# Kernel optimization log

Hardware: AMD Instinct MI355X
Metric: run time of the kernel (lower is better)

## Reference

```python
import jax, jax.numpy as jnp
import numpy as np

KNOW, ITEM, D, L, LAT, B, S = 1024, 20000, 128, 2, 256, 256, 200
NTOT = ITEM + KNOW
E1, E2 = 32768, 160000


def graph_layer(h, W, a, src, dst, n):
    # GAT-style: gather src/dst, edge MLP, segment softmax over dst, weighted scatter-sum
    z = h @ W                                              # [N, D]
    e = jax.nn.leaky_relu((jnp.concatenate([z[src], z[dst]], axis=-1) @ a)[:, 0])  # [E]
    m = jax.ops.segment_max(e, dst, num_segments=n)
    m = jnp.where(jnp.isfinite(m), m, 0.0)                 # nodes with no in-edges
    w = jnp.exp(e - m[dst])                                # [E]
    den = jax.ops.segment_sum(w, dst, num_segments=n)      # [N]
    num = jax.ops.segment_sum(w[:, None] * z[src], dst, num_segments=n)  # [N, D]
    return jnp.where(den[:, None] > 0, num / jnp.maximum(den, 1e-12)[:, None], 0.0)


def setup_inputs() -> dict:
    key = jax.random.key(0)
    ks = jax.random.split(key, 32)
    p = lambda i, shp: jax.random.normal(ks[i], shp, dtype=jnp.float32) * 0.05
    inp = {
        'p_rec': jax.random.randint(ks[0], (B, S), 0, ITEM),
        'p_target': jax.random.randint(ks[1], (B,), 0, S),
        'a_rec': jax.random.randint(ks[2], (B, S), 0, 3),
        'kn_rec': jax.random.uniform(ks[3], (B, S, KNOW), dtype=jnp.float32),
        'kn_num': jnp.ones((B, S), dtype=jnp.float32),
        'src1': jax.random.randint(ks[4], (E1,), 0, KNOW),
        'dst1': jax.random.randint(ks[5], (E1,), 0, KNOW),
        'src2': jax.random.randint(ks[6], (E2,), 0, NTOT),
        'dst2': jax.random.randint(ks[7], (E2,), 0, NTOT),
        'src3': jax.random.randint(ks[8], (E2,), 0, NTOT),
        'dst3': jax.random.randint(ks[9], (E2,), 0, NTOT),
        'kn_table': p(10, (KNOW, D)),
        'exer_table': p(11, (ITEM, D)),
        'ans_table': p(12, (3, D)),
        'gW': p(13, (L, 3, D, D)),
        'gA': p(14, (L, 3, 2 * D, 1)),
        'raW1': p(15, (L, D, D)),
        'raB1': jnp.zeros((L, D), jnp.float32),
        'raW2': p(16, (L, D, 1)),
        'actW1': p(17, (3 * D, LAT)),
        'actB1': jnp.zeros((LAT,), jnp.float32),
        'actW2': p(18, (LAT, ITEM)),
        'actB2': jnp.zeros((ITEM,), jnp.float32),
        'vW1': p(19, (3, 3 * D, LAT)),
        'vB1': jnp.zeros((3, LAT), jnp.float32),
        'vW2': p(20, (3, LAT, 1)),
        'vB2': jnp.zeros((3, 1), jnp.float32),
    }
    return inp


def reference(p_rec, p_target, a_rec, kn_rec, kn_num, src1, dst1, src2, dst2, src3, dst3,
              kn_table, exer_table, ans_table, gW, gA, raW1, raB1, raW2,
              actW1, actB1, actW2, actB2, vW1, vB1, vW2, vB2):
    kn, ex = kn_table, exer_table
    for l in range(L):  # GraphEncoder: stacked Fusion blocks (distinct params)
        k_dir = graph_layer(kn, gW[l, 0], gA[l, 0], src1, dst1, KNOW)
        ek = jnp.concatenate([ex, kn], axis=0)             # [NTOT, D]
        kfe = graph_layer(ek, gW[l, 1], gA[l, 1], src2, dst2, NTOT)
        efk = graph_layer(ek, gW[l, 2], gA[l, 2], src3, dst3, NTOT)
        A_, B_ = k_dir, kfe[ITEM:]
        ra = lambda x: jnp.tanh(x @ raW1[l] + raB1[l]) @ raW2[l]  # [KNOW, 1]
        s = jax.nn.softmax(jnp.concatenate([ra(A_), ra(B_)], axis=1), axis=1)
        kn = s[:, :1] * A_ + s[:, 1:2] * B_
        ex = efk[:ITEM]
    # hidden_layer
    be = ex[p_rec]                                         # [B, S, D]
    ba = ans_table[a_rec]                                  # [B, S, D]
    bk = jnp.einsum('bsk,kd->bsd', kn_rec, kn) / kn_num[..., None]
    item = jnp.concatenate([be, ba, bk], axis=-1)          # [B, S, 3D]
    m = (jnp.arange(S)[None, :] < (p_target + 1)[:, None]).astype(item.dtype)
    h = (item * m[..., None]).sum(axis=1) / m.sum(axis=1, keepdims=True)  # [B, 3D]
    logits = jnp.tanh(h @ actW1 + actB1) @ actW2 + actB2   # [B, ITEM]
    vh = jnp.tanh(jnp.einsum('bd,kdl->kbl', h, vW1) + vB1[:, None, :])
    vals = jnp.einsum('kbl,klo->kbo', vh, vW2) + vB2[:, None, :]  # [3, B, 1]
    return logits, vals[0], vals[1], vals[2]
```

## Files before the change

### kernel.cpp

```cpp
#include <hip/hip_runtime.h>

#define D 128
#define KNOW 1024
#define ITEM 20000
#define NTOT (ITEM + KNOW)
#define LAYERS 2
#define LAT 256
#define BB 256
#define SS 200
#define H3 (3 * D)
#define CH 4
#define ZROWS 64
#define NBK (KNOW / ZROWS)
#define NBN ((NTOT + ZROWS - 1) / ZROWS)
#define NZT (NBK + NBN)
#define NAGGU (KNOW / 4 + ITEM / 4)
#define NKROW (BB * CH)
#define XPITCH 68
#define NLOGB ((ITEM + 255) / 256)
#define NLV (NLOGB * (BB / 32))
#define NVB ((3 * BB + 3) / 4)

__global__ __launch_bounds__(256) void zdv_ker(
    const float* __restrict__ Xe, const float* __restrict__ Xk,
    const float* __restrict__ gW, const float* __restrict__ gA,
    const float* __restrict__ wa2, int layer,
    float* __restrict__ z1, float* __restrict__ z3,
    float* __restrict__ ds1, float* __restrict__ dd1,
    float* __restrict__ ds2, float* __restrict__ dd2,
    float* __restrict__ ds3, float* __restrict__ dd3)
{
    __shared__ __align__(16) float xT[D * XPITCH];
    int bid = blockIdx.x;
    int g, row0, nmax;
    if (bid < NBK) { g = 0; row0 = bid * ZROWS;          nmax = KNOW; }
    else           { g = 2; row0 = (bid - NBK) * ZROWS;  nmax = NTOT; }
    const float* W = gW + (size_t)(layer * 3 + g) * D * D;
    const float* A = gA + (size_t)(layer * 3 + g) * 2 * D;
    float* Z  = (g == 0) ? z1  : z3;
    float* DS = (g == 0) ? ds1 : ds3;
    float* DD = (g == 0) ? dd1 : dd3;

    int tid = threadIdx.x;
#pragma unroll
    for (int i = 0; i < 8; ++i) {
        int flat = tid + i * 256;
        int row  = flat >> 5;
        int f4   = flat & 31;
        int grow = row0 + row;
        float4 v = make_float4(0.f, 0.f, 0.f, 0.f);
        if (grow < nmax) {
            const float* src = (g == 0) ? (Xk + (size_t)grow * D)
                             : (grow < ITEM ? Xe + (size_t)grow * D
                                            : Xk + (size_t)(grow - ITEM) * D);
            v = *(const float4*)(src + f4 * 4);
        }
        int slot = row ^ ((f4 & 7) << 2);
        int kk = f4 * 4;
        xT[(kk + 0) * XPITCH + slot] = v.x;
        xT[(kk + 1) * XPITCH + slot] = v.y;
        xT[(kk + 2) * XPITCH + slot] = v.z;
        xT[(kk + 3) * XPITCH + slot] = v.w;
    }
    __syncthreads();

    int cg_ = tid & 31;
    int rg = tid >> 5;
    int c0 = cg_ * 4;
    int r0a = rg * 8, r0b = rg * 8 + 4;

    float acc[8][4];
#pragma unroll
    for (int r = 0; r < 8; ++r)
#pragma unroll
        for (int c = 0; c < 4; ++c) acc[r][c] = 0.f;

#pragma unroll 4
    for (int k = 0; k < D; ++k) {
        float4 wv = *(const float4*)(W + (size_t)k * D + c0);
        int xc = ((k >> 2) & 7) << 2;
        float4 xa = *(const float4*)&xT[k * XPITCH + (r0a ^ xc)];
        float4 xb = *(const float4*)&xT[k * XPITCH + (r0b ^ xc)];
        acc[0][0] = fmaf(xa.x, wv.x, acc[0][0]); acc[0][1] = fmaf(xa.x, wv.y, acc[0][1]);
        acc[0][2] = fmaf(xa.x, wv.z, acc[0][2]); acc[0][3] = fmaf(xa.x, wv.w, acc[0][3]);
        acc[1][0] = fmaf(xa.y, wv.x, acc[1][0]); acc[1][1] = fmaf(xa.y, wv.y, acc[1][1]);
        acc[1][2] = fmaf(xa.y, wv.z, acc[1][2]); acc[1][3] = fmaf(xa.y, wv.w, acc[1][3]);
        acc[2][0] = fmaf(xa.z, wv.x, acc[2][0]); acc[2][1] = fmaf(xa.z, wv.y, acc[2][1]);
        acc[2][2] = fmaf(xa.z, wv.z, acc[2][2]); acc[2][3] = fmaf(xa.z, wv.w, acc[2][3]);
        acc[3][0] = fmaf(xa.w, wv.x, acc[3][0]); acc[3][1] = fmaf(xa.w, wv.y, acc[3][1]);
        acc[3][2] = fmaf(xa.w, wv.z, acc[3][2]); acc[3][3] = fmaf(xa.w, wv.w, acc[3][3]);
        acc[4][0] = fmaf(xb.x, wv.x, acc[4][0]); acc[4][1] = fmaf(xb.x, wv.y, acc[4][1]);
        acc[4][2] = fmaf(xb.x, wv.z, acc[4][2]); acc[4][3] = fmaf(xb.x, wv.w, acc[4][3]);
        acc[5][0] = fmaf(xb.y, wv.x, acc[5][0]); acc[5][1] = fmaf(xb.y, wv.y, acc[5][1]);
        acc[5][2] = fmaf(xb.y, wv.z, acc[5][2]); acc[5][3] = fmaf(xb.y, wv.w, acc[5][3]);
        acc[6][0] = fmaf(xb.z, wv.x, acc[6][0]); acc[6][1] = fmaf(xb.z, wv.y, acc[6][1]);
        acc[6][2] = fmaf(xb.z, wv.z, acc[6][2]); acc[6][3] = fmaf(xb.z, wv.w, acc[6][3]);
        acc[7][0] = fmaf(xb.w, wv.x, acc[7][0]); acc[7][1] = fmaf(xb.w, wv.y, acc[7][1]);
        acc[7][2] = fmaf(xb.w, wv.z, acc[7][2]); acc[7][3] = fmaf(xb.w, wv.w, acc[7][3]);
    }

#pragma unroll
    for (int r = 0; r < 8; ++r) {
        int grow = row0 + ((r < 4) ? (r0a + r) : (r0b + r - 4));
        if (grow < nmax) {
            float4 v = make_float4(acc[r][0], acc[r][1], acc[r][2], acc[r][3]);
            *(float4*)(Z + (size_t)grow * D + c0) = v;
        }
    }

    float4 as = *(const float4*)(A + c0);
    float4 ad = *(const float4*)(A + D + c0);
    float ps[8], pd[8];
#pragma unroll
    for (int r = 0; r < 8; ++r) {
        ps[r] = acc[r][0] * as.x + acc[r][1] * as.y + acc[r][2] * as.z + acc[r][3] * as.w;
        pd[r] = acc[r][0] * ad.x + acc[r][1] * ad.y + acc[r][2] * ad.z + acc[r][3] * ad.w;
    }
#pragma unroll
    for (int m = 16; m; m >>= 1) {
#pragma unroll
        for (int r = 0; r < 8; ++r) {
            ps[r] += __shfl_xor(ps[r], m, 64);
            pd[r] += __shfl_xor(pd[r], m, 64);
        }
    }
    if (cg_ == 0) {
#pragma unroll
        for (int r = 0; r < 8; ++r) {
            int grow = row0 + ((r < 4) ? (r0a + r) : (r0b + r - 4));
            if (grow < nmax) { DS[grow] = ps[r]; DD[grow] = pd[r]; }
        }
    }

    if (g == 2) {
        const float* was = wa2 + (size_t)layer * 2 * D;
        float4 ws4 = *(const float4*)(was + c0);
        float4 wd4 = *(const float4*)(was + D + c0);
        int xc = ((c0 >> 2) & 7) << 2;
        float pxs[8], pxd[8];
#pragma unroll
        for (int r = 0; r < 8; ++r) {
            int rr = (r < 4) ? (r0a + r) : (r0b + r - 4);
            int sl = rr ^ xc;
            float x0 = xT[(c0 + 0) * XPITCH + sl];
            float x1 = xT[(c0 + 1) * XPITCH + sl];
            float x2 = xT[(c0 + 2) * XPITCH + sl];
            float x3 = xT[(c0 + 3) * XPITCH + sl];
            pxs[r] = x0 * ws4.x + x1 * ws4.y + x2 * ws4.z + x3 * ws4.w;
            pxd[r] = x0 * wd4.x + x1 * wd4.y + x2 * wd4.z + x3 * wd4.w;
        }
#pragma unroll
        for (int m = 16; m; m >>= 1) {
#pragma unroll
            for (int r = 0; r < 8; ++r) {
                pxs[r] += __shfl_xor(pxs[r], m, 64);
                pxd[r] += __shfl_xor(pxd[r], m, 64);
            }
        }
        if (cg_ == 0) {
#pragma unroll
            for (int r = 0; r < 8; ++r) {
                int grow = row0 + ((r < 4) ? (r0a + r) : (r0b + r - 4));
                if (grow < nmax) { ds2[grow] = pxs[r]; dd2[grow] = pxd[r]; }
            }
        }
    }
}

__global__ void hist3(const int* __restrict__ d1, const int* __restrict__ d2, const int* __restrict__ d3,
                      int E1, int E2, int* __restrict__ c1, int* __restrict__ c2, int* __restrict__ c3) {
    int i = blockIdx.x * blockDim.x + threadIdx.x;
    if (i < E1) atomicAdd(&c1[d1[i]], 1);
    else if (i < E1 + E2) { int d = d2[i - E1]; if (d >= ITEM) atomicAdd(&c2[d - ITEM], 1); }
    else if (i < E1 + 2 * E2) { int d = d3[i - E1 - E2]; if (d < ITEM) atomicAdd(&c3[d], 1); }
}

__global__ __launch_bounds__(1024) void exscan3(int* __restrict__ c1, int* __restrict__ o1,
                                                int* __restrict__ c2, int* __restrict__ o2,
                                                int* __restrict__ c3, int* __restrict__ o3,
                                                const float* __restrict__ gW, const float* __restrict__ gA,
                                                float* __restrict__ wa2) {
    int g = blockIdx.x;
    if (g == 3) {
        int t = threadIdx.x;
        if (t < 2 * 2 * D) {
            int l = t >> 8, rem = t & 255;
            int v = rem >> 7, k = rem & 127;
            const float* Wp = gW + (size_t)(l * 3 + 1) * D * D + (size_t)k * D;
            const float* ap = gA + (size_t)(l * 3 + 1) * 2 * D + v * D;
            float s = 0.f;
#pragma unroll 4
            for (int j = 0; j < D; ++j) s = fmaf(Wp[j], ap[j], s);
            wa2[(l * 2 + v) * D + k] = s;
        }
        return;
    }
    int* cnt = (g == 0) ? c1 : (g == 1 ? c2 : c3);
    int* off = (g == 0) ? o1 : (g == 1 ? o2 : o3);
    int n = (g == 2) ? ITEM : KNOW;
    int tid = threadIdx.x, lane = tid & 63, wid = tid >> 6;
    int L = (n + 1023) >> 10;
    int i0 = tid * L;
    int sum = 0;
    for (int q = 0; q < L; ++q) {
        int i = i0 + q;
        if (i < n) sum += cnt[i];
    }
    int x = sum;
#pragma unroll
    for (int d = 1; d < 64; d <<= 1) { int t = __shfl_up(x, d, 64); if (lane >= d) x += t; }
    __shared__ int ws[16];
    if (lane == 63) ws[wid] = x;
    __syncthreads();
    if (wid == 0) {
        int w = (lane < 16) ? ws[lane] : 0;
#pragma unroll
        for (int d = 1; d < 16; d <<= 1) { int t = __shfl_up(w, d, 64); if (lane >= d) w += t; }
        if (lane < 16) ws[lane] = w;
    }
    __syncthreads();
    int run = x - sum + ((wid > 0) ? ws[wid - 1] : 0);
    if (tid == 0) off[0] = 0;
    for (int q = 0; q < L; ++q) {
        int i = i0 + q;
        if (i < n) {
            int v = cnt[i];
            cnt[i] = run;
            run += v;
            off[i + 1] = run;
        }
    }
}

__global__ void scatter3(const int* __restrict__ s1, const int* __restrict__ d1,
                         const int* __restrict__ s2, const int* __restrict__ d2,
                         const int* __restrict__ s3, const int* __restrict__ d3,
                         int E1, int E2, int* __restrict__ cur1, int* __restrict__ cur2, int* __restrict__ cur3,
                         int* __restrict__ e1, int* __restrict__ e2, int* __restrict__ e3) {
    int i = blockIdx.x * blockDim.x + threadIdx.x;
    if (i < E1) { int p = atomicAdd(&cur1[d1[i]], 1); e1[p] = s1[i]; }
    else if (i < E1 + E2) { int j = i - E1; int d = d2[j]; if (d >= ITEM) { int p = atomicAdd(&cur2[d - ITEM], 1); e2[p] = s2[j]; } }
    else if (i < E1 + 2 * E2) { int j = i - E1 - E2; int d = d3[j]; if (d < ITEM) { int p = atomicAdd(&cur3[d], 1); e3[p] = s3[j]; } }
}

__device__ __forceinline__ void agg_row(const float* __restrict__ Z, const float* __restrict__ dsrc,
                                        float dd, const int* __restrict__ es, int e0, int e1,
                                        int lane, float* __restrict__ acc) {
#pragma unroll
    for (int q = 0; q < 8; ++q) acc[q] = 0.f;
    if (e1 <= e0) return;
    int eg = lane >> 4, cs = lane & 15;
    float den = 0.f;
#pragma unroll 2
    for (int e = e0 + eg; e < e1; e += 4) {
        int s = es[e];
        float t = dsrc[s] + dd;
        t = (t > 0.f) ? t : 0.01f * t;
        float w = __expf(t);
        den += w;
        const float4* zr = (const float4*)(Z + (size_t)s * D + cs * 8);
        float4 za = zr[0], zb = zr[1];
        acc[0] = fmaf(w, za.x, acc[0]); acc[1] = fmaf(w, za.y, acc[1]);
        acc[2] = fmaf(w, za.z, acc[2]); acc[3] = fmaf(w, za.w, acc[3]);
        acc[4] = fmaf(w, zb.x, acc[4]); acc[5] = fmaf(w, zb.y, acc[5]);
        acc[6] = fmaf(w, zb.z, acc[6]); acc[7] = fmaf(w, zb.w, acc[7]);
    }
#pragma unroll
    for (int m = 16; m <= 32; m <<= 1) {
        den += __shfl_xor(den, m, 64);
#pragma unroll
        for (int q = 0; q < 8; ++q) acc[q] += __shfl_xor(acc[q], m, 64);
    }
    float inv = 1.f / fmaxf(den, 1e-12f);
#pragma unroll
    for (int q = 0; q < 8; ++q) acc[q] *= inv;
}

__device__ __forceinline__ void agg_rowX(const float* __restrict__ Xe, const float* __restrict__ Xk,
                                         const float* __restrict__ dsrc, float dd,
                                         const int* __restrict__ es, int e0, int e1,
                                         int lane, float* __restrict__ acc) {
#pragma unroll
    for (int q = 0; q < 8; ++q) acc[q] = 0.f;
    if (e1 <= e0) return;
    int eg = lane >> 4, cs = lane & 15;
    float den = 0.f;
#pragma unroll 2
    for (int e = e0 + eg; e < e1; e += 4) {
        int s = es[e];
        float t = dsrc[s] + dd;
        t = (t > 0.f) ? t : 0.01f * t;
        float w = __expf(t);
        den += w;
        const float* xr = (s < ITEM) ? (Xe + (size_t)s * D) : (Xk + (size_t)(s - ITEM) * D);
        const float4* zr = (const float4*)(xr + cs * 8);
        float4 za = zr[0], zb = zr[1];
        acc[0] = fmaf(w, za.x, acc[0]); acc[1] = fmaf(w, za.y, acc[1]);
        acc[2] = fmaf(w, za.z, acc[2]); acc[3] = fmaf(w, za.w, acc[3]);
        acc[4] = fmaf(w, zb.x, acc[4]); acc[5] = fmaf(w, zb.y, acc[5]);
        acc[6] = fmaf(w, zb.z, acc[6]); acc[7] = fmaf(w, zb.w, acc[7]);
    }
#pragma unroll
    for (int m = 16; m <= 32; m <<= 1) {
        den += __shfl_xor(den, m, 64);
#pragma unroll
        for (int q = 0; q < 8; ++q) acc[q] += __shfl_xor(acc[q], m, 64);
    }
    float inv = 1.f / fmaxf(den, 1e-12f);
#pragma unroll
    for (int q = 0; q < 8; ++q) acc[q] *= inv;
}

__global__ __launch_bounds__(256) void agg3c(
    const float* __restrict__ Xe, const float* __restrict__ Xk,
    const float* __restrict__ z1, const float* __restrict__ z3,
    const float* __restrict__ ds1, const float* __restrict__ dd1,
    const float* __restrict__ ds2, const float* __restrict__ dd2,
    const float* __restrict__ ds3, const float* __restrict__ dd3,
    const int* __restrict__ off1, const int* __restrict__ es1,
    const int* __restrict__ off2, const int* __restrict__ es2,
    const int* __restrict__ off3, const int* __restrict__ es3,
    const float* __restrict__ gW1L,
    const float* __restrict__ raW1L, const float* __restrict__ raB1L,
    const float* __restrict__ raW2L, float* __restrict__ out,
    const float* __restrict__ kn_rec, const float* __restrict__ kn_num,
    const int* __restrict__ p_target, float* __restrict__ krowP)
{
    int wv = threadIdx.x >> 6, lane = threadIdx.x & 63;
    int eg = lane >> 4, cs = lane & 15;
    int u = blockIdx.x;
    if (u < KNOW / 4) {
        __shared__ float ABs[4][2][D];
        __shared__ float Bf[4][D];
        int i = u * 4 + wv;
        float accA[8], accB[8];
        agg_row(z1, ds1, dd1[i], es1, off1[i], off1[i + 1], lane, accA);
        agg_rowX(Xe, Xk, ds2, dd2[ITEM + i], es2, off2[i], off2[i + 1], lane, accB);
        if (eg == 0) {
            *(float4*)&ABs[wv][0][cs * 8]     = make_float4(accA[0], accA[1], accA[2], accA[3]);
            *(float4*)&ABs[wv][0][cs * 8 + 4] = make_float4(accA[4], accA[5], accA[6], accA[7]);
            *(float4*)&ABs[wv][1][cs * 8]     = make_float4(accB[0], accB[1], accB[2], accB[3]);
            *(float4*)&ABs[wv][1][cs * 8 + 4] = make_float4(accB[4], accB[5], accB[6], accB[7]);
        }
        __syncthreads();
        int j0 = lane * 2;
        float fB0 = 0.f, fB1 = 0.f;
#pragma unroll 4
        for (int k = 0; k < D; ++k) {
            float xv = ABs[wv][1][k];
            float2 w = *(const float2*)(gW1L + (size_t)k * D + j0);
            fB0 = fmaf(xv, w.x, fB0); fB1 = fmaf(xv, w.y, fB1);
        }
        Bf[wv][j0] = fB0; Bf[wv][j0 + 1] = fB1;
        __syncthreads();
        float b0 = raB1L[j0], b1 = raB1L[j0 + 1];
        float aA0 = b0, aA1 = b1, aB0 = b0, aB1 = b1;
#pragma unroll 4
        for (int k = 0; k < D; ++k) {
            float av = ABs[wv][0][k], bv = Bf[wv][k];
            float2 w = *(const float2*)(raW1L + (size_t)k * D + j0);
            aA0 = fmaf(av, w.x, aA0); aA1 = fmaf(av, w.y, aA1);
            aB0 = fmaf(bv, w.x, aB0); aB1 = fmaf(bv, w.y, aB1);
        }
        float2 w2 = *(const float2*)(raW2L + j0);
        float pA = tanhf(aA0) * w2.x + tanhf(aA1) * w2.y;
        float pB = tanhf(aB0) * w2.x + tanhf(aB1) * w2.y;
#pragma unroll
        for (int o = 32; o; o >>= 1) { pA += __shfl_xor(pA, o, 64); pB += __shfl_xor(pB, o, 64); }
        float mx2 = fmaxf(pA, pB);
        float eA = __expf(pA - mx2), eB = __expf(pB - mx2);
        float s = 1.f / (eA + eB);
        float sA = eA * s, sB = eB * s;
        float2 Av = *(float2*)&ABs[wv][0][j0];
        float2 Bv = make_float2(Bf[wv][j0], Bf[wv][j0 + 1]);
        *(float2*)(out + (size_t)(ITEM + i) * D + j0) =
            make_float2(sA * Av.x + sB * Bv.x, sA * Av.y + sB * Bv.y);
    } else if (u < NAGGU) {
        int row = (u - KNOW / 4) * 4 + wv;
        if (row < ITEM) {
            float acc[8];
            agg_row(z3, ds3, dd3[row], es3, off3[row], off3[row + 1], lane, acc);
            if (eg == 0) {
                *(float4*)(out + (size_t)row * D + cs * 8)     = make_float4(acc[0], acc[1], acc[2], acc[3]);
                *(float4*)(out + (size_t)row * D + cs * 8 + 4) = make_float4(acc[4], acc[5], acc[6], acc[7]);
            }
        }
    } else {
        int uk = u - NAGGU;
        int b = uk & (BB - 1), ch = uk >> 8;
        int cnt = p_target[b] + 1;
        int per = (SS + CH - 1) / CH;
        int s0 = ch * per, s1 = s0 + per;
        if (s1 > cnt) s1 = cnt;
        int k0 = threadIdx.x * 4;
        float4 a = make_float4(0.f, 0.f, 0.f, 0.f);
        for (int s = s0; s < s1; ++s) {
            float inv = 1.f / kn_num[b * SS + s];
            float4 v = *(const float4*)(kn_rec + ((size_t)b * SS + s) * KNOW + k0);
            a.x += v.x * inv; a.y += v.y * inv; a.z += v.z * inv; a.w += v.w * inv;
        }
        *(float4*)(krowP + ((size_t)ch * BB + b) * KNOW + k0) = a;
    }
}

__global__ __launch_bounds__(512) void hker(const float* __restrict__ ex, const float* __restrict__ ans_table,
                                            const int* __restrict__ p_rec, const int* __restrict__ a_rec,
                                            const int* __restrict__ p_target, const float* __restrict__ krowP,
                                            const float* __restrict__ kn, float* __restrict__ h) {
    int b = blockIdx.x;
    int j = threadIdx.x & 127, sg = threadIdx.x >> 7;
    int cnt = p_target[b] + 1;
    __shared__ int pidx[SS], aidx[SS];
    __shared__ float kr[KNOW];
    __shared__ float red[4][3][128];
    for (int i = threadIdx.x; i < cnt; i += 512) { pidx[i] = p_rec[b * SS + i]; aidx[i] = a_rec[b * SS + i]; }
    for (int i = threadIdx.x; i < KNOW; i += 512) {
        float s = 0.f;
#pragma unroll
        for (int c = 0; c < CH; ++c) s += krowP[((size_t)c * BB + b) * KNOW + i];
        kr[i] = s;
    }
    __syncthreads();
    float accE = 0.f, accA = 0.f;
    for (int s = sg; s < cnt; s += 4) {
        accE += ex[(size_t)pidx[s] * D + j];
        accA += ans_table[aidx[s] * D + j];
    }
    float accK = 0.f;
    for (int k = sg * 256; k < sg * 256 + 256; ++k) accK += kr[k] * kn[(size_t)k * D + j];
    red[sg][0][j] = accE; red[sg][1][j] = accA; red[sg][2][j] = accK;
    __syncthreads();
    if (sg == 0) {
        float inv = 1.f / (float)cnt;
        float e = (red[0][0][j] + red[1][0][j] + red[2][0][j] + red[3][0][j]) * inv;
        float a = (red[0][1][j] + red[1][1][j] + red[2][1][j] + red[3][1][j]) * inv;
        float kv = (red[0][2][j] + red[1][2][j] + red[2][2][j] + red[3][2][j]) * inv;
        h[b * H3 + j] = e;
        h[b * H3 + D + j] = a;
        h[b * H3 + 2 * D + j] = kv;
    }
}

__global__ __launch_bounds__(256) void hidden_gemm(const float* __restrict__ h,
                                                   const float* __restrict__ actW1, const float* __restrict__ actB1,
                                                   const float* __restrict__ vW1, const float* __restrict__ vB1,
                                                   float* __restrict__ hid) {
    __shared__ float hT[H3 * 17];
    int tid = threadIdx.x;
    int b0 = blockIdx.x * 16;
    for (int idx = tid; idx < 16 * H3; idx += 256) {
        int r = idx / H3, k = idx - r * H3;
        hT[k * 17 + r] = h[(size_t)(b0 + r) * H3 + k];
    }
    __syncthreads();
    int j = blockIdx.y * 64 + (tid & 63);
    int head = j >> 8, jj = j & 255;
    int rg = tid >> 6, r0 = rg * 4;
    const float* W = (head == 0) ? actW1 : (vW1 + (size_t)(head - 1) * H3 * LAT);
    float bias = (head == 0) ? actB1[jj] : vB1[(head - 1) * LAT + jj];
    float acc[4] = {bias, bias, bias, bias};
#pragma unroll 4
    for (int k = 0; k < H3; ++k) {
        float w = W[(size_t)k * LAT + jj];
        float h0 = hT[k * 17 + r0 + 0];
        float h1 = hT[k * 17 + r0 + 1];
        float h2 = hT[k * 17 + r0 + 2];
        float h3 = hT[k * 17 + r0 + 3];
        acc[0] = fmaf(h0, w, acc[0]);
        acc[1] = fmaf(h1, w, acc[1]);
        acc[2] = fmaf(h2, w, acc[2]);
        acc[3] = fmaf(h3, w, acc[3]);
    }
#pragma unroll
    for (int r = 0; r < 4; ++r)
        hid[((size_t)head * BB + (b0 + r0 + r)) * LAT + jj] = tanhf(acc[r]);
}

__global__ __launch_bounds__(256) void logitsvals(const float* __restrict__ hid,
                                                  const float* __restrict__ actW2, const float* __restrict__ actB2,
                                                  const float* __restrict__ vW2, const float* __restrict__ vB2,
                                                  float* __restrict__ out) {
    int bid = blockIdx.x;
    int tid = threadIdx.x;
    if (bid < NLV) {
        __shared__ float hT[LAT * 33];
        int ix = bid / (BB / 32), iy = bid % (BB / 32);
        int b0 = iy * 32;
        for (int idx = tid; idx < 32 * LAT; idx += 256) {
            int r = idx >> 8, k = idx & 255;
            hT[k * 33 + r] = hid[(size_t)(b0 + r) * LAT + k];
        }
        __syncthreads();
        int lane6 = tid & 63;
        int rg = tid >> 6, r0 = rg * 8;
        int ibase = ix * 256 + lane6;
        int icol[4], icl[4];
        float bias[4];
#pragma unroll
        for (int c = 0; c < 4; ++c) {
            icol[c] = ibase + c * 64;
            icl[c] = icol[c] < ITEM ? icol[c] : (ITEM - 1);
            bias[c] = actB2[icl[c]];
        }
        float acc[8][4];
#pragma unroll
        for (int r = 0; r < 8; ++r)
#pragma unroll
            for (int c = 0; c < 4; ++c) acc[r][c] = bias[c];
#pragma unroll 2
        for (int k = 0; k < LAT; ++k) {
            float w0 = actW2[(size_t)k * ITEM + icl[0]];
            float w1 = actW2[(size_t)k * ITEM + icl[1]];
            float w2 = actW2[(size_t)k * ITEM + icl[2]];
            float w3 = actW2[(size_t)k * ITEM + icl[3]];
            const float* hp = &hT[k * 33 + r0];
#pragma unroll
            for (int r = 0; r < 8; ++r) {
                float hv = hp[r];
                acc[r][0] = fmaf(hv, w0, acc[r][0]);
                acc[r][1] = fmaf(hv, w1, acc[r][1]);
                acc[r][2] = fmaf(hv, w2, acc[r][2]);
                acc[r][3] = fmaf(hv, w3, acc[r][3]);
            }
        }
#pragma unroll
        for (int c = 0; c < 4; ++c) {
            if (icol[c] < ITEM) {
#pragma unroll
                for (int r = 0; r < 8; ++r)
                    out[(size_t)(b0 + r0 + r) * ITEM + icol[c]] = acc[r][c];
            }
        }
    } else {
        int idx = (bid - NLV) * 4 + (tid >> 6);
        int lane = tid & 63;
        if (idx >= 3 * BB) return;
        int k = idx / BB, b = idx - k * BB;
        const float* vh = hid + ((size_t)(k + 1) * BB + b) * LAT;
        float4 a = ((const float4*)vh)[lane];
        float4 w = ((const float4*)(vW2 + k * LAT))[lane];
        float s = a.x * w.x + a.y * w.y + a.z * w.z + a.w * w.w;
#pragma unroll
        for (int o = 32; o; o >>= 1) s += __shfl_down(s, o, 64);
        if (lane == 0) out[(size_t)BB * ITEM + k * BB + b] = s + vB2[k];
    }
}

extern "C" void kernel_launch(void* const* d_in, const int* in_sizes, int n_in,
                              void* d_out, int out_size, void* d_ws, size_t ws_size,
                              hipStream_t stream) {
    const int*   p_rec      = (const int*)d_in[0];
    const int*   p_target   = (const int*)d_in[1];
    const int*   a_rec      = (const int*)d_in[2];
    const float* kn_rec     = (const float*)d_in[3];
    const float* kn_num     = (const float*)d_in[4];
    const int*   src1       = (const int*)d_in[5];
    const int*   dst1       = (const int*)d_in[6];
    const int*   src2       = (const int*)d_in[7];
    const int*   dst2       = (const int*)d_in[8];
    const int*   src3       = (const int*)d_in[9];
    const int*   dst3       = (const int*)d_in[10];
    const float* kn_table   = (const float*)d_in[11];
    const float* exer_table = (const float*)d_in[12];
    const float* ans_table  = (const float*)d_in[13];
    const float* gW         = (const float*)d_in[14];
    const float* gA         = (const float*)d_in[15];
    const float* raW1       = (const float*)d_in[16];
    const float* raB1       = (const float*)d_in[17];
    const float* raW2       = (const float*)d_in[18];
    const float* actW1      = (const float*)d_in[19];
    const float* actB1      = (const float*)d_in[20];
    const float* actW2      = (const float*)d_in[21];
    const float* actB2      = (const float*)d_in[22];
    const float* vW1        = (const float*)d_in[23];
    const float* vB1        = (const float*)d_in[24];
    const float* vW2        = (const float*)d_in[25];
    const float* vB2        = (const float*)d_in[26];
    const int E1 = in_sizes[5], E2 = in_sizes[7];

    float* base = (float*)d_ws;
    size_t o = 0;
    auto alloc = [&](size_t n) -> float* { float* p = base + o; o += (n + 3) & ~(size_t)3; return p; };
    float* buf0 = alloc((size_t)NTOT * D);
    float* buf1 = alloc((size_t)NTOT * D);
    float* z1   = alloc((size_t)KNOW * D);
    float* z3   = alloc((size_t)NTOT * D);
    float* ds1 = alloc(KNOW);  float* dd1 = alloc(KNOW);
    float* ds2 = alloc(NTOT);  float* dd2 = alloc(NTOT);
    float* ds3 = alloc(NTOT);  float* dd3 = alloc(NTOT);
    float* wa2 = alloc(2 * 2 * D);
    int* cnts = (int*)alloc(2 * KNOW + NTOT);
    int* cnt1 = cnts, *cnt2 = cnts + KNOW, *cnt3 = cnts + 2 * KNOW;
    int* off1 = (int*)alloc(KNOW + 1);
    int* off2 = (int*)alloc(KNOW + 1);
    int* off3 = (int*)alloc(ITEM + 1);
    int* es1  = (int*)alloc(E1);
    int* es2  = (int*)alloc(E2);
    int* es3  = (int*)alloc(E2);
    float* krowP = alloc((size_t)CH * BB * KNOW);
    float* hbuf  = alloc((size_t)BB * H3);
    float* hid   = alloc((size_t)4 * BB * LAT);

    hipMemsetAsync(cnts, 0, sizeof(int) * (2 * KNOW + NTOT), stream);

    int etot = E1 + 2 * E2;
    hist3<<<(etot + 255) / 256, 256, 0, stream>>>(dst1, dst2, dst3, E1, E2, cnt1, cnt2, cnt3);
    exscan3<<<4, 1024, 0, stream>>>(cnt1, off1, cnt2, off2, cnt3, off3, gW, gA, wa2);
    scatter3<<<(etot + 255) / 256, 256, 0, stream>>>(src1, dst1, src2, dst2, src3, dst3,
                                                     E1, E2, cnt1, cnt2, cnt3, es1, es2, es3);

    for (int l = 0; l < LAYERS; ++l) {
        const float* Xe = (l == 0) ? exer_table : buf0;
        const float* Xk = (l == 0) ? kn_table : (buf0 + (size_t)ITEM * D);
        float* out = (l == 0) ? buf0 : buf1;
        zdv_ker<<<NZT, 256, 0, stream>>>(Xe, Xk, gW, gA, wa2, l, z1, z3,
                                         ds1, dd1, ds2, dd2, ds3, dd3);
        int nb = NAGGU + ((l == 0) ? NKROW : 0);
        int reps = (l == 1) ? 2 : 1;
        for (int r = 0; r < reps; ++r)
            agg3c<<<nb, 256, 0, stream>>>(Xe, Xk, z1, z3, ds1, dd1, ds2, dd2, ds3, dd3,
                                          off1, es1, off2, es2, off3, es3,
                                          gW + (size_t)(l * 3 + 1) * D * D,
                                          raW1 + (size_t)l * D * D, raB1 + (size_t)l * D,
                                          raW2 + (size_t)l * D, out,
                                          kn_rec, kn_num, p_target, krowP);
    }

    hker<<<BB, 512, 0, stream>>>(buf1, ans_table, p_rec, a_rec, p_target, krowP, buf1 + (size_t)ITEM * D, hbuf);
    hidden_gemm<<<dim3(16, 16), 256, 0, stream>>>(hbuf, actW1, actB1, vW1, vB1, hid);
    logitsvals<<<NLV + NVB, 256, 0, stream>>>(hid, actW2, actB2, vW2, vB2, (float*)d_out);
}
```

Measured before the change: 331.2 us.

## Drop duplicate aggregation launch, split out krow kernel, widen per-lane edge gather

The second-layer aggregation kernel was launched twice with identical inputs; it now runs once per layer. The kn_rec row-reduction work that rode along in the first agg3c launch moves into its own krowk kernel, launched once after the edge scatter. The edge aggregation now has each wave process 8 edges at a time, each lane holding 16 floats instead of 8. That shortens the edge loop but doubles the accumulator registers and adds one more shuffle-reduction step. It removes a fully redundant pass over the large gather and may change occupancy.

Result: no change. 328.7 us (-0.8%).

```diff
diff --git a/kernel.cpp b/kernel.cpp
--- a/kernel.cpp
+++ b/kernel.cpp
@@ -15,7 +15,6 @@
 #define NBN ((NTOT + ZROWS - 1) / ZROWS)
 #define NZT (NBK + NBN)
 #define NAGGU (KNOW / 4 + ITEM / 4)
-#define NKROW (BB * CH)
 #define XPITCH 68
 #define NLOGB ((ITEM + 255) / 256)
 #define NLV (NLOGB * (BB / 32))
@@ -243,37 +242,57 @@
     else if (i < E1 + 2 * E2) { int j = i - E1 - E2; int d = d3[j]; if (d < ITEM) { int p = atomicAdd(&cur3[d], 1); e3[p] = s3[j]; } }
 }
 
+__global__ __launch_bounds__(256) void krowk(const float* __restrict__ kn_rec, const float* __restrict__ kn_num,
+                                             const int* __restrict__ p_target, float* __restrict__ krowP) {
+    int b = blockIdx.x, ch = blockIdx.y;
+    int cnt = p_target[b] + 1;
+    int per = (SS + CH - 1) / CH;
+    int s0 = ch * per, s1 = s0 + per;
+    if (s1 > cnt) s1 = cnt;
+    int k0 = threadIdx.x * 4;
+    float4 a = make_float4(0.f, 0.f, 0.f, 0.f);
+    for (int s = s0; s < s1; ++s) {
+        float inv = 1.f / kn_num[b * SS + s];
+        float4 v = *(const float4*)(kn_rec + ((size_t)b * SS + s) * KNOW + k0);
+        a.x += v.x * inv; a.y += v.y * inv; a.z += v.z * inv; a.w += v.w * inv;
+    }
+    *(float4*)(krowP + ((size_t)ch * BB + b) * KNOW + k0) = a;
+}
+
 __device__ __forceinline__ void agg_row(const float* __restrict__ Z, const float* __restrict__ dsrc,
                                         float dd, const int* __restrict__ es, int e0, int e1,
                                         int lane, float* __restrict__ acc) {
 #pragma unroll
-    for (int q = 0; q < 8; ++q) acc[q] = 0.f;
+    for (int q = 0; q < 16; ++q) acc[q] = 0.f;
     if (e1 <= e0) return;
-    int eg = lane >> 4, cs = lane & 15;
+    int eg = lane >> 3, cs = lane & 7;
     float den = 0.f;
-#pragma unroll 2
-    for (int e = e0 + eg; e < e1; e += 4) {
+    for (int e = e0 + eg; e < e1; e += 8) {
         int s = es[e];
         float t = dsrc[s] + dd;
         t = (t > 0.f) ? t : 0.01f * t;
         float w = __expf(t);
         den += w;
-        const float4* zr = (const float4*)(Z + (size_t)s * D + cs * 8);
-        float4 za = zr[0], zb = zr[1];
-        acc[0] = fmaf(w, za.x, acc[0]); acc[1] = fmaf(w, za.y, acc[1]);
-        acc[2] = fmaf(w, za.z, acc[2]); acc[3] = fmaf(w, za.w, acc[3]);
-        acc[4] = fmaf(w, zb.x, acc[4]); acc[5] = fmaf(w, zb.y, acc[5]);
-        acc[6] = fmaf(w, zb.z, acc[6]); acc[7] = fmaf(w, zb.w, acc[7]);
-    }
-#pragma unroll
-    for (int m = 16; m <= 32; m <<= 1) {
+        const float4* zr = (const float4*)(Z + (size_t)s * D + cs * 16);
+        float4 z0 = zr[0], z1v = zr[1], z2v = zr[2], z3v = zr[3];
+        acc[0]  = fmaf(w, z0.x,  acc[0]);  acc[1]  = fmaf(w, z0.y,  acc[1]);
+        acc[2]  = fmaf(w, z0.z,  acc[2]);  acc[3]  = fmaf(w, z0.w,  acc[3]);
+        acc[4]  = fmaf(w, z1v.x, acc[4]);  acc[5]  = fmaf(w, z1v.y, acc[5]);
+        acc[6]  = fmaf(w, z1v.z, acc[6]);  acc[7]  = fmaf(w, z1v.w, acc[7]);
+        acc[8]  = fmaf(w, z2v.x, acc[8]);  acc[9]  = fmaf(w, z2v.y, acc[9]);
+        acc[10] = fmaf(w, z2v.z, acc[10]); acc[11] = fmaf(w, z2v.w, acc[11]);
+        acc[12] = fmaf(w, z3v.x, acc[12]); acc[13] = fmaf(w, z3v.y, acc[13]);
+        acc[14] = fmaf(w, z3v.z, acc[14]); acc[15] = fmaf(w, z3v.w, acc[15]);
+    }
+#pragma unroll
+    for (int m = 8; m <= 32; m <<= 1) {
         den += __shfl_xor(den, m, 64);
 #pragma unroll
-        for (int q = 0; q < 8; ++q) acc[q] += __shfl_xor(acc[q], m, 64);
+        for (int q = 0; q < 16; ++q) acc[q] += __shfl_xor(acc[q], m, 64);
     }
     float inv = 1.f / fmaxf(den, 1e-12f);
 #pragma unroll
-    for (int q = 0; q < 8; ++q) acc[q] *= inv;
+    for (int q = 0; q < 16; ++q) acc[q] *= inv;
 }
 
 __device__ __forceinline__ void agg_rowX(const float* __restrict__ Xe, const float* __restrict__ Xk,
@@ -281,34 +300,37 @@
                                          const int* __restrict__ es, int e0, int e1,
                                          int lane, float* __restrict__ acc) {
 #pragma unroll
-    for (int q = 0; q < 8; ++q) acc[q] = 0.f;
+    for (int q = 0; q < 16; ++q) acc[q] = 0.f;
     if (e1 <= e0) return;
-    int eg = lane >> 4, cs = lane & 15;
+    int eg = lane >> 3, cs = lane & 7;
     float den = 0.f;
-#pragma unroll 2
-    for (int e = e0 + eg; e < e1; e += 4) {
+    for (int e = e0 + eg; e < e1; e += 8) {
         int s = es[e];
         float t = dsrc[s] + dd;
         t = (t > 0.f) ? t : 0.01f * t;
         float w = __expf(t);
         den += w;
         const float* xr = (s < ITEM) ? (Xe + (size_t)s * D) : (Xk + (size_t)(s - ITEM) * D);
-        const float4* zr = (const float4*)(xr + cs * 8);
-        float4 za = zr[0], zb = zr[1];
-        acc[0] = fmaf(w, za.x, acc[0]); acc[1] = fmaf(w, za.y, acc[1]);
-        acc[2] = fmaf(w, za.z, acc[2]); acc[3] = fmaf(w, za.w, acc[3]);
-        acc[4] = fmaf(w, zb.x, acc[4]); acc[5] = fmaf(w, zb.y, acc[5]);
-        acc[6] = fmaf(w, zb.z, acc[6]); acc[7] = fmaf(w, zb.w, acc[7]);
-    }
-#pragma unroll
-    for (int m = 16; m <= 32; m <<= 1) {
+        const float4* zr = (const float4*)(xr + cs * 16);
+        float4 z0 = zr[0], z1v = zr[1], z2v = zr[2], z3v = zr[3];
+        acc[0]  = fmaf(w, z0.x,  acc[0]);  acc[1]  = fmaf(w, z0.y,  acc[1]);
+        acc[2]  = fmaf(w, z0.z,  acc[2]);  acc[3]  = fmaf(w, z0.w,  acc[3]);
+        acc[4]  = fmaf(w, z1v.x, acc[4]);  acc[5]  = fmaf(w, z1v.y, acc[5]);
+        acc[6]  = fmaf(w, z1v.z, acc[6]);  acc[7]  = fmaf(w, z1v.w, acc[7]);
+        acc[8]  = fmaf(w, z2v.x, acc[8]);  acc[9]  = fmaf(w, z2v.y, acc[9]);
+        acc[10] = fmaf(w, z2v.z, acc[10]); acc[11] = fmaf(w, z2v.w, acc[11]);
+        acc[12] = fmaf(w, z3v.x, acc[12]); acc[13] = fmaf(w, z3v.y, acc[13]);
+        acc[14] = fmaf(w, z3v.z, acc[14]); acc[15] = fmaf(w, z3v.w, acc[15]);
+    }
+#pragma unroll
+    for (int m = 8; m <= 32; m <<= 1) {
         den += __shfl_xor(den, m, 64);
 #pragma unroll
-        for (int q = 0; q < 8; ++q) acc[q] += __shfl_xor(acc[q], m, 64);
+        for (int q = 0; q < 16; ++q) acc[q] += __shfl_xor(acc[q], m, 64);
     }
     float inv = 1.f / fmaxf(den, 1e-12f);
 #pragma unroll
-    for (int q = 0; q < 8; ++q) acc[q] *= inv;
+    for (int q = 0; q < 16; ++q) acc[q] *= inv;
 }
 
 __global__ __launch_bounds__(256) void agg3c(
@@ -322,25 +344,26 @@
     const int* __restrict__ off3, const int* __restrict__ es3,
     const float* __restrict__ gW1L,
     const float* __restrict__ raW1L, const float* __restrict__ raB1L,
-    const float* __restrict__ raW2L, float* __restrict__ out,
-    const float* __restrict__ kn_rec, const float* __restrict__ kn_num,
-    const int* __restrict__ p_target, float* __restrict__ krowP)
+    const float* __restrict__ raW2L, float* __restrict__ out)
 {
     int wv = threadIdx.x >> 6, lane = threadIdx.x & 63;
-    int eg = lane >> 4, cs = lane & 15;
+    int eg = lane >> 3, cs = lane & 7;
     int u = blockIdx.x;
     if (u < KNOW / 4) {
         __shared__ float ABs[4][2][D];
         __shared__ float Bf[4][D];
         int i = u * 4 + wv;
-        float accA[8], accB[8];
+        float accA[16], accB[16];
         agg_row(z1, ds1, dd1[i], es1, off1[i], off1[i + 1], lane, accA);
         agg_rowX(Xe, Xk, ds2, dd2[ITEM + i], es2, off2[i], off2[i + 1], lane, accB);
         if (eg == 0) {
-            *(float4*)&ABs[wv][0][cs * 8]     = make_float4(accA[0], accA[1], accA[2], accA[3]);
-            *(float4*)&ABs[wv][0][cs * 8 + 4] = make_float4(accA[4], accA[5], accA[6], accA[7]);
-            *(float4*)&ABs[wv][1][cs * 8]     = make_float4(accB[0], accB[1], accB[2], accB[3]);
-            *(float4*)&ABs[wv][1][cs * 8 + 4] = make_float4(accB[4], accB[5], accB[6], accB[7]);
+#pragma unroll
+            for (int q4 = 0; q4 < 4; ++q4) {
+                *(float4*)&ABs[wv][0][cs * 16 + q4 * 4] =
+                    make_float4(accA[q4 * 4], accA[q4 * 4 + 1], accA[q4 * 4 + 2], accA[q4 * 4 + 3]);
+                *(float4*)&ABs[wv][1][cs * 16 + q4 * 4] =
+                    make_float4(accB[q4 * 4], accB[q4 * 4 + 1], accB[q4 * 4 + 2], accB[q4 * 4 + 3]);
+            }
         }
         __syncthreads();
         int j0 = lane * 2;
@@ -375,31 +398,18 @@
         float2 Bv = make_float2(Bf[wv][j0], Bf[wv][j0 + 1]);
         *(float2*)(out + (size_t)(ITEM + i) * D + j0) =
             make_float2(sA * Av.x + sB * Bv.x, sA * Av.y + sB * Bv.y);
-    } else if (u < NAGGU) {
+    } else {
         int row = (u - KNOW / 4) * 4 + wv;
         if (row < ITEM) {
-            float acc[8];
+            float acc[16];
             agg_row(z3, ds3, dd3[row], es3, off3[row], off3[row + 1], lane, acc);
             if (eg == 0) {
-                *(float4*)(out + (size_t)row * D + cs * 8)     = make_float4(acc[0], acc[1], acc[2], acc[3]);
-                *(float4*)(out + (size_t)row * D + cs * 8 + 4) = make_float4(acc[4], acc[5], acc[6], acc[7]);
+#pragma unroll
+                for (int q4 = 0; q4 < 4; ++q4)
+                    *(float4*)(out + (size_t)row * D + cs * 16 + q4 * 4) =
+                        make_float4(acc[q4 * 4], acc[q4 * 4 + 1], acc[q4 * 4 + 2], acc[q4 * 4 + 3]);
             }
         }
-    } else {
-        int uk = u - NAGGU;
-        int b = uk & (BB - 1), ch = uk >> 8;
-        int cnt = p_target[b] + 1;
-        int per = (SS + CH - 1) / CH;
-        int s0 = ch * per, s1 = s0 + per;
-        if (s1 > cnt) s1 = cnt;
-        int k0 = threadIdx.x * 4;
-        float4 a = make_float4(0.f, 0.f, 0.f, 0.f);
-        for (int s = s0; s < s1; ++s) {
-            float inv = 1.f / kn_num[b * SS + s];
-            float4 v = *(const float4*)(kn_rec + ((size_t)b * SS + s) * KNOW + k0);
-            a.x += v.x * inv; a.y += v.y * inv; a.z += v.z * inv; a.w += v.w * inv;
-        }
-        *(float4*)(krowP + ((size_t)ch * BB + b) * KNOW + k0) = a;
     }
 }
 
@@ -608,6 +618,7 @@
     exscan3<<<4, 1024, 0, stream>>>(cnt1, off1, cnt2, off2, cnt3, off3, gW, gA, wa2);
     scatter3<<<(etot + 255) / 256, 256, 0, stream>>>(src1, dst1, src2, dst2, src3, dst3,
                                                      E1, E2, cnt1, cnt2, cnt3, es1, es2, es3);
+    krowk<<<dim3(BB, CH), 256, 0, stream>>>(kn_rec, kn_num, p_target, krowP);
 
     for (int l = 0; l < LAYERS; ++l) {
         const float* Xe = (l == 0) ? exer_table : buf0;
@@ -615,15 +626,11 @@
         float* out = (l == 0) ? buf0 : buf1;
         zdv_ker<<<NZT, 256, 0, stream>>>(Xe, Xk, gW, gA, wa2, l, z1, z3,
                                          ds1, dd1, ds2, dd2, ds3, dd3);
-        int nb = NAGGU + ((l == 0) ? NKROW : 0);
-        int reps = (l == 1) ? 2 : 1;
-        for (int r = 0; r < reps; ++r)
-            agg3c<<<nb, 256, 0, stream>>>(Xe, Xk, z1, z3, ds1, dd1, ds2, dd2, ds3, dd3,
-                                          off1, es1, off2, es2, off3, es3,
-                                          gW + (size_t)(l * 3 + 1) * D * D,
-                                          raW1 + (size_t)l * D * D, raB1 + (size_t)l * D,
-                                          raW2 + (size_t)l * D, out,
-                                          kn_rec, kn_num, p_target, krowP);
+        agg3c<<<NAGGU, 256, 0, stream>>>(Xe, Xk, z1, z3, ds1, dd1, ds2, dd2, ds3, dd3,
+                                         off1, es1, off2, es2, off3, es3,
+                                         gW + (size_t)(l * 3 + 1) * D * D,
+                                         raW1 + (size_t)l * D * D, raB1 + (size_t)l * D,
+                                         raW2 + (size_t)l * D, out);
     }
 
     hker<<<BB, 512, 0, stream>>>(buf1, ans_table, p_rec, a_rec, p_target, krowP, buf1 + (size_t)ITEM * D, hbuf);
```
